# Kernel tuning notes

Measured on AMD Instinct MI355X. Metric: run time of the kernel, lower is better.

The kernel has to match this reference:

```python
import jax, jax.numpy as jnp
import numpy as np

# Straight-through-estimator round (round_pass in the original code)
def _round_ste(x):
    return x + jax.lax.stop_gradient(jnp.round(x) - x)

INPUT_QMAX = 127.0   # 2**(input_bit-1)-1,  input_bit=8
WEIGHT_QMAX = 127.0  # 2**(weight_bit-1)-1, weight_bit=8
OUT_RANGE = 127.0    # 2**(output_bit-1)-1, output_bit=8


def setup_inputs() -> dict:
    key = jax.random.key(0)
    k0, k1, k2 = jax.random.split(key, 3)
    B, Cin, Cout, H, W, K = 16, 320, 320, 64, 64, 3
    x = jax.random.normal(k0, (B, Cin, H, W), dtype=jnp.float32)
    weight = jax.random.normal(k1, (Cout, Cin, K, K), dtype=jnp.float32) * 0.05
    bias = jax.random.normal(k2, (Cout,), dtype=jnp.float32) * 0.1
    # LSQ learned scalar step sizes (cloned from conv_lsq in the original)
    step_x = jnp.float32(0.02)
    step_w = jnp.float32(0.002)
    step_b = jnp.float32(0.01)
    # Bit_shift_layer scale: shift conv accumulator down into output_bit range
    shift_scale = jnp.float32(2.0 ** -7)
    return {"x": x, "weight": weight, "bias": bias, "step_x": step_x,
            "step_w": step_w, "step_b": step_b, "shift_scale": shift_scale}


def reference(x, weight, bias, step_x, step_w, step_b, shift_scale):
    # --- lsq_quant_input (isint=True): x_int in [-127,127], x_scale = 1/step ---
    x_int = jnp.clip(_round_ste(x / step_x), -INPUT_QMAX, INPUT_QMAX)
    x_scale = 1.0 / step_x
    # --- lsq_quant_weight (isint=True) ---
    w_int = jnp.clip(_round_ste(weight / step_w), -WEIGHT_QMAX, WEIGHT_QMAX)
    w_scale = 1.0 / step_w
    # --- Conv2d_int: integer-valued conv (no bias) ---
    y_int = jax.lax.conv_general_dilated(
        x_int, w_int, window_strides=(1, 1), padding=((1, 1), (1, 1)),
        dimension_numbers=("NCHW", "OIHW", "NCHW"))
    # --- mvm_result_shift: bit-shift accumulator into output range ---
    y_shift = jnp.clip(_round_ste(y_int * shift_scale), -OUT_RANGE, OUT_RANGE)
    # --- lsq_quant_bias (isint=False): dequantized bias ---
    b_deq = jnp.clip(_round_ste(bias / step_b), -OUT_RANGE, OUT_RANGE) * step_b
    # --- bias requant to output int scale, add, clamp (fused epilogue) ---
    b_int8 = jnp.clip(_round_ste(b_deq * shift_scale * x_scale * w_scale),
                      -OUT_RANGE, OUT_RANGE)
    y_shift_dmac = jnp.clip(y_shift + b_int8[None, :, None, None],
                            -OUT_RANGE, OUT_RANGE)
    # module returns y_shift_DMAC (the integer-valued clamped output)
    return y_shift_dmac
```

## Files before the change

### kernel.cpp

```cpp
#include <hip/hip_runtime.h>

typedef int v4i __attribute__((ext_vector_type(4)));

#define QMAX 127.0f

#define XQ_BYTES 22302720
#define WQ_BYTES 921600

__device__ __forceinline__ float clampf(float v, float lo, float hi) {
    return fminf(fmaxf(v, lo), hi);
}

__device__ __forceinline__ float qround(float v, float step, float inv) {
    float t = v * inv;
    float r = rintf(t);
    float d = fabsf(t - r);
    if (fabsf(d - 0.5f) < fabsf(t) * 1e-5f + 1e-5f)
        r = rintf(v / step);
    return r;
}

__device__ __forceinline__ void gload_lds16(const char* g, char* l) {
    __builtin_amdgcn_global_load_lds(
        (const __attribute__((address_space(1))) void*)g,
        (__attribute__((address_space(3))) void*)l, 16, 0, 0);
}

__device__ __forceinline__ v4i mfma_i8(v4i a, v4i b, v4i c) {
    return __builtin_amdgcn_mfma_i32_16x16x64_i8(a, b, c, 0, 0, 0);
}

__global__ __launch_bounds__(256) void quant_x_kernel(
    const float* __restrict__ x, const float* __restrict__ step_p,
    char* __restrict__ xq)
{
    __shared__ float F[64 * 65];
    const int t = threadIdx.x;
    const int h = blockIdx.x;
    const int b = blockIdx.y;
    const float step = *step_p;
    const float inv  = 1.0f / step;
    const int w  = t >> 2;
    const int cg = t & 3;
    v4i vals[5];

    for (int c5 = 0; c5 < 5; ++c5) {
        {
            const int r = t >> 4, c = (t & 15) * 4;
            const float* src = x + (((size_t)(b * 320 + c5 * 64) * 64 + h) * 64);
#pragma unroll
            for (int i = 0; i < 4; ++i) {
                const int row = r + i * 16;
                *(float4*)&F[row * 65 + c] =
                    *(const float4*)(src + (size_t)row * 4096 + c);
            }
        }
        __syncthreads();
        int dws[4];
#pragma unroll
        for (int j = 0; j < 4; ++j) {
            int word = 0;
#pragma unroll
            for (int k = 0; k < 4; ++k) {
                float v = F[(cg * 16 + j * 4 + k) * 65 + w];
                int xi = (int)clampf(qround(v, step, inv), -QMAX, QMAX);
                word |= (xi & 0xFF) << (8 * k);
            }
            dws[j] = word;
        }
        vals[c5] = (v4i){dws[0], dws[1], dws[2], dws[3]};
        __syncthreads();
    }

    const int col = w + 1;
    const int key = (col >> 1) & 3;
    char* base = xq + ((size_t)(b * 66 + (h + 1)) * 66 + col) * 320;
#pragma unroll
    for (int c5 = 0; c5 < 5; ++c5)
        *(v4i*)(base + c5 * 64 + (((cg ^ key)) << 4)) = vals[c5];
}

__global__ __launch_bounds__(256) void prep_kernel(
    const float* __restrict__ w, const float* __restrict__ bias,
    const float* __restrict__ step_w_p, const float* __restrict__ step_b_p,
    const float* __restrict__ step_x_p, const float* __restrict__ shift_p,
    char* __restrict__ wq2, char* __restrict__ xq, float* __restrict__ bi)
{
    const int bid = blockIdx.x;
    if (bid < 3600) {
        const int tid = bid * 256 + threadIdx.x;
        const float step = *step_w_p;
        const float inv  = 1.0f / step;
        const int p    = tid / 102400;
        const int r    = tid - p * 102400;
        const int c5   = r / 20480;
        const int r2   = r - c5 * 20480;
        const int cog  = r2 >> 10;
        const int r3   = r2 & 1023;
        const int lane = r3 >> 4, j = r3 & 15;
        const int co = cog * 16 + (lane & 15);
        const int ci = c5 * 64 + (lane >> 4) * 16 + j;
        float v = w[(size_t)co * 2880 + ci * 9 + p];
        int q = (int)clampf(qround(v, step, inv), -QMAX, QMAX);
        wq2[tid] = (char)q;
    } else if (bid < 3925) {
        int tid = (bid - 3600) * 256 + threadIdx.x;
        if (tid < 83200) {
            int b = tid / 5200;
            int r = tid - b * 5200;
            int px = r / 20;
            int ck = (r - px * 20) * 16;
            int row, col;
            if (px < 66)       { row = 0;  col = px; }
            else if (px < 132) { row = 65; col = px - 66; }
            else { int e = px - 132; row = 1 + (e >> 1); col = (e & 1) * 65; }
            size_t off = ((size_t)(b * 66 + row) * 66 + col) * 320 + ck;
            v4i z = {0, 0, 0, 0};
            *(v4i*)&xq[off] = z;
        }
    } else {
        const float step_b = *step_b_p;
        const float xs = 1.0f / *step_x_p;
        const float ws = 1.0f / *step_w_p;
        const float shift = *shift_p;
#pragma unroll
        for (int co = threadIdx.x; co < 320; co += 256) {
            float b_deq = clampf(rintf(bias[co] / step_b), -QMAX, QMAX) * step_b;
            float v = ((b_deq * shift) * xs) * ws;
            bi[co] = clampf(rintf(v), -QMAX, QMAX);
        }
    }
}

__global__ __launch_bounds__(256, 3) void conv_mfma_kernel(
    const char* __restrict__ xq, const char* __restrict__ wq2,
    const float* __restrict__ bi, const float* __restrict__ shift_p,
    float* __restrict__ out)
{
    __shared__ __attribute__((aligned(16))) char B_lds[2][25344];

    const int t   = threadIdx.x;
    const int bx  = blockIdx.x;
    const int co0 = bx * 64;
    const int ptile = blockIdx.y;
    const int b  = ptile >> 4;
    const int h0 = (ptile & 15) * 4;

    const int wave = t >> 6, lane = t & 63;
    const int quad = lane >> 4, l15 = lane & 15;

    const char* xbase = xq + ((size_t)(b * 66 + h0) * 66) * 320;

    v4i acc[4][4] = {};

    for (int c = t; c < 1584; c += 256) {
        const char* g = xbase + (c >> 2) * 320 + ((c & 3) << 4);
        gload_lds16(g, &B_lds[0][(c - lane) * 16]);
    }
    __syncthreads();

    for (int c5 = 0; c5 < 5; ++c5) {
        if (c5 < 4) {
            const int ci0 = (c5 + 1) * 64;
            char* dst = B_lds[(c5 + 1) & 1];
            for (int c = t; c < 1584; c += 256) {
                const char* g = xbase + (c >> 2) * 320 + ci0 + ((c & 3) << 4);
                gload_lds16(g, &dst[(c - lane) * 16]);
            }
        }

        const char* Bc = B_lds[c5 & 1];
        const char* wp = wq2 + (c5 * 20 + bx * 4) * 1024 + lane * 16;

#pragma unroll
        for (int p = 0; p < 9; ++p) {
            const int dh = p / 3, dw = p - dh * 3;
            v4i a[4];
#pragma unroll
            for (int cs = 0; cs < 4; ++cs)
                a[cs] = *(const v4i*)(wp + p * 102400 + cs * 1024);
            const int prow = wave + dh;
#pragma unroll
            for (int i = 0; i < 4; ++i) {
                const int col = i * 16 + l15 + dw;
                const int key = (col >> 1) & 3;
                v4i bf = *(const v4i*)&Bc[(prow * 66 + col) * 64 +
                                          ((quad ^ key) << 4)];
#pragma unroll
                for (int cs = 0; cs < 4; ++cs)
                    acc[cs][i] = mfma_i8(a[cs], bf, acc[cs][i]);
            }
        }
        __syncthreads();
    }

    const float shift = *shift_p;
    const int h = h0 + wave;
#pragma unroll
    for (int cs = 0; cs < 4; ++cs) {
#pragma unroll
        for (int reg = 0; reg < 4; ++reg) {
            const int co = co0 + cs * 16 + quad * 4 + reg;
            const float bv = bi[co];
            float* orow = out + (((size_t)(b * 320 + co) * 64) + h) * 64;
#pragma unroll
            for (int i = 0; i < 4; ++i) {
                float y  = (float)acc[cs][i][reg];
                float ys = clampf(rintf(y * shift), -QMAX, QMAX);
                orow[i * 16 + l15] = clampf(ys + bv, -QMAX, QMAX);
            }
        }
    }
}

extern "C" void kernel_launch(void* const* d_in, const int* in_sizes, int n_in,
                              void* d_out, int out_size, void* d_ws, size_t ws_size,
                              hipStream_t stream) {
    const float* x      = (const float*)d_in[0];
    const float* w      = (const float*)d_in[1];
    const float* bias   = (const float*)d_in[2];
    const float* step_x = (const float*)d_in[3];
    const float* step_w = (const float*)d_in[4];
    const float* step_b = (const float*)d_in[5];
    const float* shift  = (const float*)d_in[6];
    float* out = (float*)d_out;

    char*  xq  = (char*)d_ws;
    char*  wq2 = xq + XQ_BYTES;
    float* bi  = (float*)(wq2 + WQ_BYTES);

    quant_x_kernel<<<dim3(64, 16), 256, 0, stream>>>(x, step_x, xq);
    prep_kernel<<<3926, 256, 0, stream>>>(w, bias, step_w, step_b, step_x, shift,
                                          wq2, xq, bi);
    conv_mfma_kernel<<<dim3(5, 256), 256, 0, stream>>>(xq, wq2, bi, shift, out);
}
```

Before: 226.1 us.

## Fuse prep kernels, swizzle conv block order, and software-pipeline weight and LDS loads

The x-quantization and weight/bias/padding prep kernels are merged into one launch, removing a kernel boundary and letting the two phases share the GPU. The conv grid becomes 1-D with a remapping that groups eight pixel tiles per output-channel block, aiming for better L2 reuse of input tiles across the five channel blocks. Inside the conv loop, the weight fragments for the next tap are prefetched into a double-buffered register set and LDS B reads are issued one step ahead. s_setprio is raised around the MFMA bursts. This increases register pressure under the 3-blocks-per-SM launch bound.

```diff
diff --git a/kernel.cpp b/kernel.cpp
--- a/kernel.cpp
+++ b/kernel.cpp
@@ -30,65 +30,63 @@
     return __builtin_amdgcn_mfma_i32_16x16x64_i8(a, b, c, 0, 0, 0);
 }
 
-__global__ __launch_bounds__(256) void quant_x_kernel(
-    const float* __restrict__ x, const float* __restrict__ step_p,
-    char* __restrict__ xq)
+__global__ __launch_bounds__(256) void fused_prep_kernel(
+    const float* __restrict__ x, const float* __restrict__ w,
+    const float* __restrict__ bias,
+    const float* __restrict__ step_x_p, const float* __restrict__ step_w_p,
+    const float* __restrict__ step_b_p, const float* __restrict__ shift_p,
+    char* __restrict__ xq, char* __restrict__ wq2, float* __restrict__ bi)
 {
     __shared__ float F[64 * 65];
+    const int bid = blockIdx.x;
     const int t = threadIdx.x;
-    const int h = blockIdx.x;
-    const int b = blockIdx.y;
-    const float step = *step_p;
-    const float inv  = 1.0f / step;
-    const int w  = t >> 2;
-    const int cg = t & 3;
-    v4i vals[5];
-
-    for (int c5 = 0; c5 < 5; ++c5) {
-        {
-            const int r = t >> 4, c = (t & 15) * 4;
-            const float* src = x + (((size_t)(b * 320 + c5 * 64) * 64 + h) * 64);
-#pragma unroll
-            for (int i = 0; i < 4; ++i) {
-                const int row = r + i * 16;
-                *(float4*)&F[row * 65 + c] =
-                    *(const float4*)(src + (size_t)row * 4096 + c);
-            }
-        }
-        __syncthreads();
-        int dws[4];
-#pragma unroll
-        for (int j = 0; j < 4; ++j) {
-            int word = 0;
-#pragma unroll
-            for (int k = 0; k < 4; ++k) {
-                float v = F[(cg * 16 + j * 4 + k) * 65 + w];
-                int xi = (int)clampf(qround(v, step, inv), -QMAX, QMAX);
-                word |= (xi & 0xFF) << (8 * k);
-            }
-            dws[j] = word;
-        }
-        vals[c5] = (v4i){dws[0], dws[1], dws[2], dws[3]};
-        __syncthreads();
-    }
-
-    const int col = w + 1;
-    const int key = (col >> 1) & 3;
-    char* base = xq + ((size_t)(b * 66 + (h + 1)) * 66 + col) * 320;
-#pragma unroll
-    for (int c5 = 0; c5 < 5; ++c5)
-        *(v4i*)(base + c5 * 64 + (((cg ^ key)) << 4)) = vals[c5];
-}
-
-__global__ __launch_bounds__(256) void prep_kernel(
-    const float* __restrict__ w, const float* __restrict__ bias,
-    const float* __restrict__ step_w_p, const float* __restrict__ step_b_p,
-    const float* __restrict__ step_x_p, const float* __restrict__ shift_p,
-    char* __restrict__ wq2, char* __restrict__ xq, float* __restrict__ bi)
-{
-    const int bid = blockIdx.x;
-    if (bid < 3600) {
-        const int tid = bid * 256 + threadIdx.x;
+
+    if (bid < 1024) {
+        const int h = bid & 63;
+        const int b = bid >> 6;
+        const float step = *step_x_p;
+        const float inv  = 1.0f / step;
+        const int wcol = t >> 2;
+        const int cg   = t & 3;
+        v4i vals[5];
+
+        for (int c5 = 0; c5 < 5; ++c5) {
+            {
+                const int r = t >> 4, c = (t & 15) * 4;
+                const float* src = x + (((size_t)(b * 320 + c5 * 64) * 64 + h) * 64);
+#pragma unroll
+                for (int i = 0; i < 4; ++i) {
+                    const int row = r + i * 16;
+                    *(float4*)&F[row * 65 + c] =
+                        *(const float4*)(src + (size_t)row * 4096 + c);
+                }
+            }
+            __syncthreads();
+            int dws[4];
+#pragma unroll
+            for (int j = 0; j < 4; ++j) {
+                int word = 0;
+#pragma unroll
+                for (int k = 0; k < 4; ++k) {
+                    float v = F[(cg * 16 + j * 4 + k) * 65 + wcol];
+                    int xi = (int)clampf(qround(v, step, inv), -QMAX, QMAX);
+                    word |= (xi & 0xFF) << (8 * k);
+                }
+                dws[j] = word;
+            }
+            vals[c5] = (v4i){dws[0], dws[1], dws[2], dws[3]};
+            __syncthreads();
+        }
+
+        const int col = wcol + 1;
+        const int key = (col >> 1) & 3;
+        char* base = xq + ((size_t)(b * 66 + (h + 1)) * 66 + col) * 320;
+#pragma unroll
+        for (int c5 = 0; c5 < 5; ++c5)
+            *(v4i*)(base + c5 * 64 + (((cg ^ key)) << 4)) = vals[c5];
+
+    } else if (bid < 4624) {
+        const int tid = (bid - 1024) * 256 + t;
         const float step = *step_w_p;
         const float inv  = 1.0f / step;
         const int p    = tid / 102400;
@@ -103,8 +101,8 @@
         float v = w[(size_t)co * 2880 + ci * 9 + p];
         int q = (int)clampf(qround(v, step, inv), -QMAX, QMAX);
         wq2[tid] = (char)q;
-    } else if (bid < 3925) {
-        int tid = (bid - 3600) * 256 + threadIdx.x;
+    } else if (bid < 4949) {
+        int tid = (bid - 4624) * 256 + t;
         if (tid < 83200) {
             int b = tid / 5200;
             int r = tid - b * 5200;
@@ -124,7 +122,7 @@
         const float ws = 1.0f / *step_w_p;
         const float shift = *shift_p;
 #pragma unroll
-        for (int co = threadIdx.x; co < 320; co += 256) {
+        for (int co = t; co < 320; co += 256) {
             float b_deq = clampf(rintf(bias[co] / step_b), -QMAX, QMAX) * step_b;
             float v = ((b_deq * shift) * xs) * ws;
             bi[co] = clampf(rintf(v), -QMAX, QMAX);
@@ -139,10 +137,14 @@
 {
     __shared__ __attribute__((aligned(16))) char B_lds[2][25344];
 
-    const int t   = threadIdx.x;
-    const int bx  = blockIdx.x;
+    const int t  = threadIdx.x;
+    const int id = blockIdx.x;
+    const int g  = id / 40;
+    const int r  = id - g * 40;
+    const int bx = r >> 3;
+    const int ptile = (g << 3) | (r & 7);
+
     const int co0 = bx * 64;
-    const int ptile = blockIdx.y;
     const int b  = ptile >> 4;
     const int h0 = (ptile & 15) * 4;
 
@@ -154,8 +156,8 @@
     v4i acc[4][4] = {};
 
     for (int c = t; c < 1584; c += 256) {
-        const char* g = xbase + (c >> 2) * 320 + ((c & 3) << 4);
-        gload_lds16(g, &B_lds[0][(c - lane) * 16]);
+        const char* gp = xbase + (c >> 2) * 320 + ((c & 3) << 4);
+        gload_lds16(gp, &B_lds[0][(c - lane) * 16]);
     }
     __syncthreads();
 
@@ -164,31 +166,45 @@
             const int ci0 = (c5 + 1) * 64;
             char* dst = B_lds[(c5 + 1) & 1];
             for (int c = t; c < 1584; c += 256) {
-                const char* g = xbase + (c >> 2) * 320 + ci0 + ((c & 3) << 4);
-                gload_lds16(g, &dst[(c - lane) * 16]);
+                const char* gp = xbase + (c >> 2) * 320 + ci0 + ((c & 3) << 4);
+                gload_lds16(gp, &dst[(c - lane) * 16]);
             }
         }
 
         const char* Bc = B_lds[c5 & 1];
         const char* wp = wq2 + (c5 * 20 + bx * 4) * 1024 + lane * 16;
 
+        v4i areg[2][4];
+#pragma unroll
+        for (int cs = 0; cs < 4; ++cs)
+            areg[0][cs] = *(const v4i*)(wp + 0 * 102400 + cs * 1024);
+
 #pragma unroll
         for (int p = 0; p < 9; ++p) {
             const int dh = p / 3, dw = p - dh * 3;
-            v4i a[4];
-#pragma unroll
-            for (int cs = 0; cs < 4; ++cs)
-                a[cs] = *(const v4i*)(wp + p * 102400 + cs * 1024);
+            if (p < 8) {
+#pragma unroll
+                for (int cs = 0; cs < 4; ++cs)
+                    areg[(p + 1) & 1][cs] =
+                        *(const v4i*)(wp + (p + 1) * 102400 + cs * 1024);
+            }
             const int prow = wave + dh;
-#pragma unroll
-            for (int i = 0; i < 4; ++i) {
+            auto bread = [&](int i) -> v4i {
                 const int col = i * 16 + l15 + dw;
                 const int key = (col >> 1) & 3;
-                v4i bf = *(const v4i*)&Bc[(prow * 66 + col) * 64 +
-                                          ((quad ^ key) << 4)];
+                return *(const v4i*)&Bc[(prow * 66 + col) * 64 +
+                                        ((quad ^ key) << 4)];
+            };
+            v4i bf = bread(0);
+#pragma unroll
+            for (int i = 0; i < 4; ++i) {
+                v4i bcur = bf;
+                if (i < 3) bf = bread(i + 1);
+                __builtin_amdgcn_s_setprio(1);
 #pragma unroll
                 for (int cs = 0; cs < 4; ++cs)
-                    acc[cs][i] = mfma_i8(a[cs], bf, acc[cs][i]);
+                    acc[cs][i] = mfma_i8(areg[p & 1][cs], bcur, acc[cs][i]);
+                __builtin_amdgcn_s_setprio(0);
             }
         }
         __syncthreads();
@@ -229,8 +245,7 @@
     char*  wq2 = xq + XQ_BYTES;
     float* bi  = (float*)(wq2 + WQ_BYTES);
 
-    quant_x_kernel<<<dim3(64, 16), 256, 0, stream>>>(x, step_x, xq);
-    prep_kernel<<<3926, 256, 0, stream>>>(w, bias, step_w, step_b, step_x, shift,
-                                          wq2, xq, bi);
-    conv_mfma_kernel<<<dim3(5, 256), 256, 0, stream>>>(xq, wq2, bi, shift, out);
-}
+    fused_prep_kernel<<<4950, 256, 0, stream>>>(x, w, bias, step_x, step_w,
+                                                step_b, shift, xq, wq2, bi);
+    conv_mfma_kernel<<<1280, 256, 0, stream>>>(xq, wq2, bi, shift, out);
+}
```

Measured after the change: 209.8 us. -7.2%, faster.
